# Optimization experiments

Hardware: AMD Instinct MI355X
Metric: run time of the kernel (lower is better)

## Reference

```python
import math
import jax, jax.numpy as jnp
import numpy as np

B, T, F = 2, 1024, 1024
H, DK, DV = 16, 64, 64
OUT = 1024


def _rel_shift_left(x):
    # x: (b, h, t1, t2); Transformer-XL left shift + tril mask (causal part)
    b, h, t1, t2 = x.shape
    xp = jnp.pad(x, ((0, 0), (0, 0), (0, 0), (1, 0)))
    xp = xp.reshape(b, h, t2 + 1, t1)[:, :, 1:].reshape(b, h, t1, t2)
    tril = jnp.tril(jnp.ones((t1, t2), x.dtype), t2 - t1)
    return xp * tril


def _rel_shift_right(x):
    # x: (b, h, t1, t2); right shift + triu mask (non-causal part)
    b, h, t1, t2 = x.shape
    xp = jnp.pad(x, ((0, 0), (0, 0), (0, 0), (0, 1)))
    xp = xp.reshape(b, h, t2 + 1, t1)[:, :, :-1].reshape(b, h, t1, t2)
    triu = jnp.triu(jnp.ones((t1, t2), x.dtype), t2 - t1 + 1)
    return xp * triu


def setup_inputs() -> dict:
    key = jax.random.key(0)
    ks = jax.random.split(key, 16)
    s = 0.02
    return {
        'query': jax.random.normal(ks[0], (B, T, F), jnp.float32),
        'key': jax.random.normal(ks[1], (B, T, F), jnp.float32),
        'value': jax.random.normal(ks[2], (B, T, F), jnp.float32),
        'pos_emb': jax.random.normal(ks[3], (1, T, F), jnp.float32),
        'Wq': jax.random.normal(ks[4], (H * DK, F), jnp.float32) * s,
        'bq': jnp.zeros((H * DK,), jnp.float32),
        'Wk': jax.random.normal(ks[5], (H * DK, F), jnp.float32) * s,
        'bk': jnp.zeros((H * DK,), jnp.float32),
        'Wv': jax.random.normal(ks[6], (H * DV, F), jnp.float32) * s,
        'bv': jnp.zeros((H * DV,), jnp.float32),
        'Wp': jax.random.normal(ks[7], (H * DK, F), jnp.float32) * s,
        'bp': jnp.zeros((H * DK,), jnp.float32),
        'Wo': jax.random.normal(ks[8], (OUT, H * DV), jnp.float32) * s,
        'bo': jnp.zeros((OUT,), jnp.float32),
        'u_bias': jax.random.normal(ks[9], (H, DK), jnp.float32) * s,
        'v_bias': jax.random.normal(ks[10], (H, DK), jnp.float32) * s,
    }


def reference(query, key, value, pos_emb, Wq, bq, Wk, bk, Wv, bv, Wp, bp, Wo, bo, u_bias, v_bias):
    b, t1, _ = query.shape
    t2 = key.shape[1]
    q = (query @ Wq.T + bq).reshape(b, t1, H, DK)          # (b, t1, h, dk)
    k = (key @ Wk.T + bk).reshape(b, t2, H, DK).transpose(0, 2, 1, 3)   # (b, h, t2, dk)
    v = (value @ Wv.T + bv).reshape(b, t2, H, DV).transpose(0, 2, 1, 3) # (b, h, t2, dv)
    p = (pos_emb @ Wp.T + bp).reshape(pos_emb.shape[0], -1, H, DK).transpose(0, 2, 1, 3)[0]  # (h, t2, dk)

    q_plus_u = (q + u_bias).transpose(0, 2, 1, 3)  # (b, h, t1, dk)
    q_plus_v = (q + v_bias).transpose(0, 2, 1, 3)  # (b, h, t1, dk)

    AC = jnp.einsum('bhtd,bhsd->bhts', q_plus_u, k)
    BD = _rel_shift_left(jnp.einsum('bhtd,hsd->bhts', q_plus_v, p))
    # non-causal part: flip pos embeddings along time, right shift
    BD = BD + _rel_shift_right(jnp.einsum('bhtd,hsd->bhts', q_plus_v, jnp.flip(p, axis=1)))

    scores = (AC + BD) / math.sqrt(DK)
    attn = jax.nn.softmax(scores, axis=-1)
    x = jnp.einsum('bhts,bhsd->bthd', attn, v).reshape(b, t1, H * DV)
    return x @ Wo.T + bo
```

## Files before the change

### kernel.cpp

```cpp
#include <hip/hip_runtime.h>
#include <hip/hip_bf16.h>
#include <stdint.h>

typedef __attribute__((ext_vector_type(8))) short bf16x8;
typedef __attribute__((ext_vector_type(4))) float f32x4;
typedef __attribute__((ext_vector_type(4))) short short4v;

#define SCALE2 0.18033688011112042f

__device__ __forceinline__ short f2b(float f) {
  union { float f; unsigned u; } un; un.f = f;
  unsigned r = un.u + 0x7FFFu + ((un.u >> 16) & 1u);
  return (short)(r >> 16);
}
__device__ __forceinline__ float b2f(short s) {
  union { unsigned u; float f; } un; un.u = ((unsigned)(unsigned short)s) << 16;
  return un.f;
}

#define GLDS(GP, LP) __builtin_amdgcn_global_load_lds( \
    (__attribute__((address_space(1))) void*)(GP), \
    (__attribute__((address_space(3))) void*)(LP), 16, 0, 0)

struct CvtTab { const float* s[12]; short* d[12]; };

__global__ void cvt_all(CvtTab tab) {
  int chunk = blockIdx.x >> 10;
  int off = (blockIdx.x & 1023) * 256 + threadIdx.x;
  float4 v = *((const float4*)tab.s[chunk] + off);
  short4v o;
  o[0] = f2b(v.x); o[1] = f2b(v.y); o[2] = f2b(v.z); o[3] = f2b(v.w);
  *((short4v*)tab.d[chunk] + off) = o;
}

__device__ __forceinline__ void gemm_core128(
    const short* __restrict__ A, const short* __restrict__ W,
    int tile_m, int tile_n, short* lds, f32x4 acc[4][4])
{
  const int tid = threadIdx.x;
  const int wave = tid >> 6, lane = tid & 63;
  const int wr = wave >> 1, wc = wave & 1;
  const int q15 = lane & 15, q4 = lane >> 4;
  const int rl = lane >> 3;
  const int cswz = ((lane & 7) * 16) ^ (rl << 4);

#pragma unroll
  for (int i = 0; i < 4; ++i)
#pragma unroll
    for (int j = 0; j < 4; ++j) acc[i][j] = (f32x4){0.f, 0.f, 0.f, 0.f};

  auto stage = [&](int buf, int k0) {
    short* As = lds + buf * 16384;
    short* Bs = As + 8192;
#pragma unroll
    for (int s = 0; s < 4; ++s) {
      int ia = wave * 4 + s;
      int row = ia * 8 + rl;
      GLDS(A + (size_t)(tile_m + row) * 1024 + k0 + (cswz >> 1), (char*)As + ia * 1024);
      GLDS(W + (size_t)(tile_n + row) * 1024 + k0 + (cswz >> 1), (char*)Bs + ia * 1024);
    }
  };

  stage(0, 0);
  __syncthreads();
  for (int t = 0; t < 16; ++t) {
    const int cur = t & 1;
    if (t < 15) stage(cur ^ 1, (t + 1) * 64);
    const short* As = lds + cur * 16384;
    const short* Bs = As + 8192;
#pragma unroll
    for (int kk = 0; kk < 2; ++kk) {
      const int kbyte = kk * 64 + q4 * 16;
      const int rswz = (q15 & 7) << 4;
      bf16x8 af[4], bfr[4];
#pragma unroll
      for (int i = 0; i < 4; ++i)
        af[i] = *(const bf16x8*)((const char*)As + (wr * 64 + i * 16 + q15) * 128 + (kbyte ^ rswz));
#pragma unroll
      for (int j = 0; j < 4; ++j)
        bfr[j] = *(const bf16x8*)((const char*)Bs + (wc * 64 + j * 16 + q15) * 128 + (kbyte ^ rswz));
#pragma unroll
      for (int i = 0; i < 4; ++i)
#pragma unroll
        for (int j = 0; j < 4; ++j)
          acc[i][j] = __builtin_amdgcn_mfma_f32_16x16x32_bf16(af[i], bfr[j], acc[i][j], 0, 0, 0);
    }
    __syncthreads();
  }
}

__global__ __launch_bounds__(256)
void gemm_qkvp(const short* __restrict__ q_in, const short* __restrict__ k_in,
               const short* __restrict__ v_in, const short* __restrict__ p_in,
               const short* __restrict__ wq, const short* __restrict__ wk,
               const short* __restrict__ wv, const short* __restrict__ wp,
               const float* __restrict__ bq, const float* __restrict__ bk,
               const float* __restrict__ bv, const float* __restrict__ bp,
               const float* __restrict__ ub, const float* __restrict__ vb,
               short* __restrict__ qu, short* __restrict__ qv,
               short* __restrict__ kx, short* __restrict__ vtp, short* __restrict__ pp)
{
  __shared__ __align__(16) short lds[32768];
  const int n = blockIdx.x;
  const int by = n & 7;
  const int bx = n >> 3;
  const short* A; const short* W; const float* bias; int tm, mode;
  if (bx < 16)      { A = q_in; W = wq; bias = bq; tm = bx;      mode = 0; }
  else if (bx < 32) { A = k_in; W = wk; bias = bk; tm = bx - 16; mode = 1; }
  else if (bx < 48) { A = v_in; W = wv; bias = bv; tm = bx - 32; mode = 2; }
  else              { A = p_in; W = wp; bias = bp; tm = bx - 48; mode = 3; }

  f32x4 acc[4][4];
  gemm_core128(A, W, tm * 128, by * 128, lds, acc);

  const int lane = threadIdx.x & 63, wave = threadIdx.x >> 6;
  const int wr = wave >> 1, wc = wave & 1, q15 = lane & 15, q4 = lane >> 4;
#pragma unroll
  for (int i = 0; i < 4; ++i)
#pragma unroll
    for (int j = 0; j < 4; ++j)
#pragma unroll
      for (int r = 0; r < 4; ++r) {
        int m = tm * 128 + wr * 64 + i * 16 + q4 * 4 + r;
        int nn = by * 128 + wc * 64 + j * 16 + q15;
        float v = acc[i][j][r] + bias[nn];
        int bb = m >> 10, t = m & 1023, hh = nn >> 6, d = nn & 63;
        if (mode == 0) {
          size_t o = ((size_t)(bb * 16 + hh) * 1024 + t) * 64 + d;
          qu[o] = f2b((v + ub[nn]) * SCALE2);
          qv[o] = f2b((v + vb[nn]) * SCALE2);
        } else if (mode == 1) {
          kx[((size_t)(bb * 16 + hh) * 1024 + t) * 64 + d] = f2b(v);
        } else if (mode == 2) {
          vtp[((size_t)(bb * 16 + hh) * 64 + d) * 1024 + t] = f2b(v);
        } else {
          pp[((size_t)hh * 1024 + m) * 64 + d] = f2b(v);
        }
      }
}

__global__ __launch_bounds__(256)
void gemm_out(const short* __restrict__ X, const short* __restrict__ W,
              const float* __restrict__ bo, float* __restrict__ out)
{
  __shared__ __align__(16) short lds[24576];
  const int n = blockIdx.x;
  const int bxm = (n >> 3) & 15;
  const int byn = ((n & 7) << 1) | (n >> 7);
  const int tile_m = bxm * 128, tile_n = byn * 64;

  const int tid = threadIdx.x;
  const int wave = tid >> 6, lane = tid & 63;
  const int wr = wave >> 1, wc = wave & 1;
  const int q15 = lane & 15, q4 = lane >> 4;
  const int rl = lane >> 3;
  const int cswz = ((lane & 7) * 16) ^ (rl << 4);

  f32x4 acc[4][2];
#pragma unroll
  for (int i = 0; i < 4; ++i)
#pragma unroll
    for (int j = 0; j < 2; ++j) acc[i][j] = (f32x4){0.f, 0.f, 0.f, 0.f};

  auto stage = [&](int buf, int k0) {
    short* As = lds + buf * 12288;
    short* Bs = As + 8192;
#pragma unroll
    for (int s = 0; s < 6; ++s) {
      int idx = wave * 6 + s;
      if (idx < 16) {
        int row = idx * 8 + rl;
        GLDS(X + (size_t)(tile_m + row) * 1024 + k0 + (cswz >> 1), (char*)As + idx * 1024);
      } else {
        int i2 = idx - 16;
        int row = i2 * 8 + rl;
        GLDS(W + (size_t)(tile_n + row) * 1024 + k0 + (cswz >> 1), (char*)Bs + i2 * 1024);
      }
    }
  };

  stage(0, 0);
  __syncthreads();
  for (int t = 0; t < 16; ++t) {
    const int cur = t & 1;
    if (t < 15) stage(cur ^ 1, (t + 1) * 64);
    const short* As = lds + cur * 12288;
    const short* Bs = As + 8192;
#pragma unroll
    for (int kk = 0; kk < 2; ++kk) {
      const int kbyte = kk * 64 + q4 * 16;
      const int rswz = (q15 & 7) << 4;
      bf16x8 af[4], bfr[2];
#pragma unroll
      for (int i = 0; i < 4; ++i)
        af[i] = *(const bf16x8*)((const char*)As + (wr * 64 + i * 16 + q15) * 128 + (kbyte ^ rswz));
#pragma unroll
      for (int j = 0; j < 2; ++j)
        bfr[j] = *(const bf16x8*)((const char*)Bs + (wc * 32 + j * 16 + q15) * 128 + (kbyte ^ rswz));
#pragma unroll
      for (int i = 0; i < 4; ++i)
#pragma unroll
        for (int j = 0; j < 2; ++j)
          acc[i][j] = __builtin_amdgcn_mfma_f32_16x16x32_bf16(af[i], bfr[j], acc[i][j], 0, 0, 0);
    }
    __syncthreads();
  }

#pragma unroll
  for (int i = 0; i < 4; ++i)
#pragma unroll
    for (int j = 0; j < 2; ++j)
#pragma unroll
      for (int r = 0; r < 4; ++r) {
        int m = tile_m + wr * 64 + i * 16 + q4 * 4 + r;
        int nn = tile_n + wc * 32 + j * 16 + q15;
        out[(size_t)m * 1024 + nn] = acc[i][j][r] + bo[nn];
      }
}

__global__ __launch_bounds__(256, 4)
void attn_kernel(const short* __restrict__ qu, const short* __restrict__ qv,
                 const short* __restrict__ kmat, const short* __restrict__ vt,
                 const short* __restrict__ p,
                 float* __restrict__ Opart, float* __restrict__ larr)
{
  __shared__ __align__(16) short Ks[4096];
  __shared__ __align__(16) short Vs[4096];
  __shared__ __align__(16) short Bl[4 * 2048];
  __shared__ __align__(16) short Pl[4 * 1024];

  const int nB = blockIdx.x;
  const int o = (nB & 7) * 128 + (nB >> 3);
  const int t0 = (o & 15) * 64;
  const int h = (o >> 4) & 15;
  const int z = o >> 8;
  const int b = z >> 1, sh = z & 1;

  const int tid = threadIdx.x;
  const int wave = tid >> 6, lane = tid & 63;
  const int q15 = lane & 15, q4 = lane >> 4;
  const size_t bh = (size_t)(b * 16 + h);
  const short* pW = p + (size_t)h * 65536;
  const int rswz = (q15 & 7) << 4;
  char* BlW = (char*)Bl + wave * 4096;
  char* PlW = (char*)Pl + wave * 2048;

  const int srow = tid >> 3;
  const int scol = (tid & 7) * 8;
  const int sdst = srow * 128 + ((scol * 2) ^ ((srow & 7) << 4));

  const int sbeg = sh * 512, send = sbeg + 512;
  const short* kg = kmat + (bh * 1024 + sbeg + srow) * 64 + scol;
  const short* vg = vt + (bh * 64 + srow) * 1024 + sbeg + scol;

  bf16x8 quf[2], qvf[2];
  {
    size_t base = (bh * 1024 + t0 + wave * 16 + q15) * 64 + q4 * 8;
    quf[0] = *(const bf16x8*)(qu + base);
    quf[1] = *(const bf16x8*)(qu + base + 32);
    qvf[0] = *(const bf16x8*)(qv + base);
    qvf[1] = *(const bf16x8*)(qv + base + 32);
  }

  f32x4 acco[4];
#pragma unroll
  for (int g = 0; g < 4; ++g) acco[g] = (f32x4){0.f, 0.f, 0.f, 0.f};
  float lrun[4] = {0.f, 0.f, 0.f, 0.f};

  int live0 = -1, live1 = -1;

  auto refill = [&](int base) {
    f32x4 bacc[4];
#pragma unroll
    for (int g = 0; g < 4; ++g) bacc[g] = (f32x4){0.f, 0.f, 0.f, 0.f};
#pragma unroll
    for (int kc = 0; kc < 2; ++kc) {
      const int kof = kc * 32 + q4 * 8;
#pragma unroll
      for (int g = 0; g < 4; ++g) {
        bf16x8 pf = *(const bf16x8*)(pW + (size_t)(base + g * 16 + q15) * 64 + kof);
        bacc[g] = __builtin_amdgcn_mfma_f32_16x16x32_bf16(qvf[kc], pf, bacc[g], 0, 0, 0);
      }
    }
#pragma unroll
    for (int g = 0; g < 4; ++g)
#pragma unroll
      for (int r = 0; r < 4; ++r) {
        int phys = ((base & 64) + g * 16 + q15 + q4 * 16) & 127;
        *(short*)(BlW + (q4 * 4 + r) * 256 + phys * 2) = f2b(bacc[g][r]);
      }
  };

  bf16x8 kr0 = *(const bf16x8*)kg;
  bf16x8 kr1 = *(const bf16x8*)(kg + 2048);
  bf16x8 vr0 = *(const bf16x8*)vg;
  bf16x8 vr1 = *(const bf16x8*)(vg + 32768);

  for (int s0 = sbeg; s0 < send; s0 += 64) {
    __syncthreads();
    *(bf16x8*)((char*)Ks + sdst) = kr0;
    *(bf16x8*)((char*)Ks + sdst + 4096) = kr1;
    *(bf16x8*)((char*)Vs + sdst) = vr0;
    *(bf16x8*)((char*)Vs + sdst + 4096) = vr1;
    __syncthreads();
    if (s0 + 64 < send) {
      kg += 4096; vg += 64;
      kr0 = *(const bf16x8*)kg;
      kr1 = *(const bf16x8*)(kg + 2048);
      vr0 = *(const bf16x8*)vg;
      vr1 = *(const bf16x8*)(vg + 32768);
    }

    f32x4 accac[4];
#pragma unroll
    for (int g = 0; g < 4; ++g) accac[g] = (f32x4){0.f, 0.f, 0.f, 0.f};
#pragma unroll
    for (int kc = 0; kc < 2; ++kc) {
      const int kbyte = kc * 64 + q4 * 16;
#pragma unroll
      for (int g = 0; g < 4; ++g) {
        bf16x8 kf = *(const bf16x8*)((const char*)Ks + (g * 16 + q15) * 128 + (kbyte ^ rswz));
        accac[g] = __builtin_amdgcn_mfma_f32_16x16x32_bf16(quf[kc], kf, accac[g], 0, 0, 0);
      }
    }

    const int dist0 = (t0 > s0) ? (t0 - s0) : (s0 - t0);
    const int jbase = 960 - dist0;
    {
      int sl = (jbase >> 6) & 1;
      bool nd = sl ? (live1 != jbase) : (live0 != jbase);
      if (nd) { refill(jbase); if (sl) live1 = jbase; else live0 = jbase; }
      int b1 = jbase + 64;
      if (b1 <= 960) {
        int sl1 = sl ^ 1;
        bool nd1 = sl1 ? (live1 != b1) : (live0 != b1);
        if (nd1) { refill(b1); if (sl1) live1 = b1; else live0 = b1; }
      }
    }

    const int rb = q4 * 1024;
    unsigned pb[4][4];
#define SCORE_ELEM(g, r, ARG) do {                                          \
      int aw = (ARG) & 127;                                                 \
      float bd = b2f(*(const short*)(BlW + rb + (r) * 256 + aw * 2));       \
      float e_ = exp2f(accac[g][r] + bd);                                   \
      unsigned t_ = __float_as_uint(e_) >> 16;                              \
      pb[g][r] = t_;                                                        \
      lrun[r] += __uint_as_float(t_ << 16);                                 \
    } while (0)

    if (s0 < t0) {
      const int C = 1023 - dist0 - wave * 16 + 12 * q4 + q15;
#pragma unroll
      for (int g = 0; g < 4; ++g)
#pragma unroll
        for (int r = 0; r < 4; ++r) SCORE_ELEM(g, r, C + 16 * g - r);
    } else if (s0 > t0) {
      const int C = 1023 - dist0 + wave * 16 + 20 * q4 - q15;
#pragma unroll
      for (int g = 0; g < 4; ++g)
#pragma unroll
        for (int r = 0; r < 4; ++r) SCORE_ELEM(g, r, C + r - 16 * g);
    } else {
      const int e0 = wave * 16 + 4 * q4 - q15;
      const int A = 1023 + 16 * q4;
#pragma unroll
      for (int g = 0; g < 4; ++g)
#pragma unroll
        for (int r = 0; r < 4; ++r) {
          int e = e0 + r - 16 * g;
          int d = e < 0 ? -e : e;
          SCORE_ELEM(g, r, A - d);
        }
    }
#undef SCORE_ELEM

#pragma unroll
    for (int g = 0; g < 4; ++g)
#pragma unroll
      for (int r = 0; r < 4; ++r) {
        int locR = q4 * 4 + r;
        *(short*)(PlW + locR * 128 + (((g * 16 + q15) * 2) ^ ((locR & 7) << 4))) = (short)pb[g][r];
      }

#pragma unroll
    for (int kc = 0; kc < 2; ++kc) {
      const int kbyte = kc * 64 + q4 * 16;
      bf16x8 pf = *(const bf16x8*)((const char*)PlW + q15 * 128 + (kbyte ^ rswz));
#pragma unroll
      for (int g = 0; g < 4; ++g) {
        bf16x8 vf = *(const bf16x8*)((const char*)Vs + (g * 16 + q15) * 128 + (kbyte ^ rswz));
        acco[g] = __builtin_amdgcn_mfma_f32_16x16x32_bf16(pf, vf, acco[g], 0, 0, 0);
      }
    }
  }

#pragma unroll
  for (int m = 1; m < 16; m <<= 1)
#pragma unroll
    for (int r = 0; r < 4; ++r) lrun[r] += __shfl_xor(lrun[r], m);

  size_t obase = ((size_t)(sh * 2 + b) * 16 + h) * 1024;
#pragma unroll
  for (int g = 0; g < 4; ++g)
#pragma unroll
    for (int r = 0; r < 4; ++r) {
      int tt = t0 + wave * 16 + q4 * 4 + r;
      Opart[(obase + tt) * 64 + g * 16 + q15] = acco[g][r];
    }
  if (q15 == 0)
#pragma unroll
    for (int r = 0; r < 4; ++r) {
      int tt = t0 + wave * 16 + q4 * 4 + r;
      larr[obase + tt] = lrun[r];
    }
}

__global__ void combine_k(const float* __restrict__ O, const float* __restrict__ larr,
                          short* __restrict__ x)
{
  int i = blockIdx.x * 256 + threadIdx.x;
  int dv4 = i & 15, rest = i >> 4;
  float4 a0 = *(const float4*)(O + (size_t)rest * 64 + dv4 * 4);
  float4 a1 = *(const float4*)(O + 2097152 + (size_t)rest * 64 + dv4 * 4);
  float l0 = larr[rest], l1 = larr[32768 + rest];
  float inv = 1.0f / (l0 + l1);
  int bq = rest >> 14, hq = (rest >> 10) & 15, tq = rest & 1023;
  short4v o;
  o[0] = f2b((a0.x + a1.x) * inv);
  o[1] = f2b((a0.y + a1.y) * inv);
  o[2] = f2b((a0.z + a1.z) * inv);
  o[3] = f2b((a0.w + a1.w) * inv);
  *(short4v*)(x + ((size_t)(bq * 1024 + tq) * 1024 + hq * 64 + dv4 * 4)) = o;
}

extern "C" void kernel_launch(void* const* d_in, const int* in_sizes, int n_in,
                              void* d_out, int out_size, void* d_ws, size_t ws_size,
                              hipStream_t stream) {
  const float* query = (const float*)d_in[0];
  const float* key   = (const float*)d_in[1];
  const float* value = (const float*)d_in[2];
  const float* pos   = (const float*)d_in[3];
  const float* Wq = (const float*)d_in[4];  const float* bq = (const float*)d_in[5];
  const float* Wk = (const float*)d_in[6];  const float* bk = (const float*)d_in[7];
  const float* Wv = (const float*)d_in[8];  const float* bv = (const float*)d_in[9];
  const float* Wp = (const float*)d_in[10]; const float* bp = (const float*)d_in[11];
  const float* Wo = (const float*)d_in[12]; const float* bo = (const float*)d_in[13];
  const float* ub = (const float*)d_in[14]; const float* vb = (const float*)d_in[15];

  char* ws = (char*)d_ws;
  const size_t MB = 1 << 20;
  short* Wo_bf    = (short*)(ws);
  short* qu_bf    = (short*)(ws + 2 * MB);
  short* qv_bf    = (short*)(ws + 6 * MB);
  short* k_bf     = (short*)(ws + 10 * MB);
  short* vT_bf    = (short*)(ws + 14 * MB);
  short* p_bf     = (short*)(ws + 18 * MB);
  short* x_bf     = (short*)(ws + 20 * MB);
  short* query_bf = (short*)(ws + 24 * MB);
  short* key_bf   = (short*)(ws + 28 * MB);
  short* value_bf = (short*)(ws + 32 * MB);
  short* pos_bf   = (short*)(ws + 36 * MB);
  short* Wq_bf    = (short*)(ws + 38 * MB);
  short* Wk_bf    = (short*)(ws + 40 * MB);
  short* Wv_bf    = (short*)(ws + 42 * MB);
  short* Wp_bf    = (short*)(ws + 44 * MB);
  float* Opart = (float*)(ws + 24 * MB);
  float* larr  = (float*)(ws + 40 * MB);

  CvtTab tab;
  tab.s[0] = query;           tab.d[0] = query_bf;
  tab.s[1] = query + 1048576; tab.d[1] = query_bf + 1048576;
  tab.s[2] = key;             tab.d[2] = key_bf;
  tab.s[3] = key + 1048576;   tab.d[3] = key_bf + 1048576;
  tab.s[4] = value;           tab.d[4] = value_bf;
  tab.s[5] = value + 1048576; tab.d[5] = value_bf + 1048576;
  tab.s[6] = pos;             tab.d[6] = pos_bf;
  tab.s[7] = Wq;              tab.d[7] = Wq_bf;
  tab.s[8] = Wk;              tab.d[8] = Wk_bf;
  tab.s[9] = Wv;              tab.d[9] = Wv_bf;
  tab.s[10] = Wp;             tab.d[10] = Wp_bf;
  tab.s[11] = Wo;             tab.d[11] = Wo_bf;
  hipLaunchKernelGGL(cvt_all, dim3(12288), dim3(256), 0, stream, tab);

  hipLaunchKernelGGL(gemm_qkvp, dim3(448), dim3(256), 0, stream,
                     query_bf, key_bf, value_bf, pos_bf,
                     Wq_bf, Wk_bf, Wv_bf, Wp_bf,
                     bq, bk, bv, bp, ub, vb,
                     qu_bf, qv_bf, k_bf, vT_bf, p_bf);

  hipLaunchKernelGGL(attn_kernel, dim3(1024), dim3(256), 0, stream,
                     qu_bf, qv_bf, k_bf, vT_bf, p_bf, Opart, larr);

  hipLaunchKernelGGL(combine_k, dim3(2048), dim3(256), 0, stream,
                     Opart, larr, x_bf);

  hipLaunchKernelGGL(gemm_out, dim3(256), dim3(256), 0, stream,
                     x_bf, Wo_bf, bo, (float*)d_out);
}
```

Baseline: 129.7 us.

## Transpose attention MFMA operands, vectorize BD/P LDS traffic, compute row sums via MFMA

Swaps the A/B operands of the score, BD-refill and PV MFMAs so each lane holds a query row across four consecutive key columns. This lets the BD table and P tile be written and read with packed 32/64-bit swizzled LDS accesses instead of per-element 16-bit ones. The softmax denominator is now accumulated by an extra MFMA against a ones vector, which removes the scalar per-element adds and the cross-lane shuffle reduction. The output is stored as float4 vectors, and s_setprio hints are wrapped around the MFMA sections. The new parity-based unaligned bf16 extraction adds ALU work and is a source of indexing risk.

Result: faster. 116.7 us (-10.0%).

```diff
diff --git a/kernel.cpp b/kernel.cpp
--- a/kernel.cpp
+++ b/kernel.cpp
@@ -5,6 +5,7 @@
 typedef __attribute__((ext_vector_type(8))) short bf16x8;
 typedef __attribute__((ext_vector_type(4))) float f32x4;
 typedef __attribute__((ext_vector_type(4))) short short4v;
+typedef __attribute__((ext_vector_type(2))) unsigned u32x2;
 
 #define SCALE2 0.18033688011112042f
 
@@ -12,10 +13,6 @@
   union { float f; unsigned u; } un; un.f = f;
   unsigned r = un.u + 0x7FFFu + ((un.u >> 16) & 1u);
   return (short)(r >> 16);
-}
-__device__ __forceinline__ float b2f(short s) {
-  union { unsigned u; float f; } un; un.u = ((unsigned)(unsigned short)s) << 16;
-  return un.f;
 }
 
 #define GLDS(GP, LP) __builtin_amdgcn_global_load_lds( \
@@ -226,8 +223,8 @@
 {
   __shared__ __align__(16) short Ks[4096];
   __shared__ __align__(16) short Vs[4096];
-  __shared__ __align__(16) short Bl[4 * 2048];
-  __shared__ __align__(16) short Pl[4 * 1024];
+  __shared__ __align__(16) short Bl[8192];
+  __shared__ __align__(16) short Pl[4096];
 
   const int nB = blockIdx.x;
   const int o = (nB & 7) * 128 + (nB >> 3);
@@ -244,6 +241,8 @@
   const int rswz = (q15 & 7) << 4;
   char* BlW = (char*)Bl + wave * 4096;
   char* PlW = (char*)Pl + wave * 2048;
+  const int blrow = q15 * 256;
+  const int plrow = q15 * 128;
 
   const int srow = tid >> 3;
   const int scol = (tid & 7) * 8;
@@ -261,11 +260,14 @@
     qvf[0] = *(const bf16x8*)(qv + base);
     qvf[1] = *(const bf16x8*)(qv + base + 32);
   }
-
-  f32x4 acco[4];
+  bf16x8 ones;
+#pragma unroll
+  for (int i = 0; i < 8; ++i) ones[i] = (short)0x3F80;
+
+  f32x4 acco[4], accl;
 #pragma unroll
   for (int g = 0; g < 4; ++g) acco[g] = (f32x4){0.f, 0.f, 0.f, 0.f};
-  float lrun[4] = {0.f, 0.f, 0.f, 0.f};
+  accl = (f32x4){0.f, 0.f, 0.f, 0.f};
 
   int live0 = -1, live1 = -1;
 
@@ -279,16 +281,22 @@
 #pragma unroll
       for (int g = 0; g < 4; ++g) {
         bf16x8 pf = *(const bf16x8*)(pW + (size_t)(base + g * 16 + q15) * 64 + kof);
-        bacc[g] = __builtin_amdgcn_mfma_f32_16x16x32_bf16(qvf[kc], pf, bacc[g], 0, 0, 0);
-      }
-    }
-#pragma unroll
-    for (int g = 0; g < 4; ++g)
-#pragma unroll
-      for (int r = 0; r < 4; ++r) {
-        int phys = ((base & 64) + g * 16 + q15 + q4 * 16) & 127;
-        *(short*)(BlW + (q4 * 4 + r) * 256 + phys * 2) = f2b(bacc[g][r]);
-      }
+        bacc[g] = __builtin_amdgcn_mfma_f32_16x16x32_bf16(pf, qvf[kc], bacc[g], 0, 0, 0);
+      }
+    }
+    const int pbase = base & 127;
+#pragma unroll
+    for (int g = 0; g < 4; ++g) {
+      unsigned a0 = __float_as_uint(bacc[g][0]); a0 = a0 + 0x7FFFu + ((a0 >> 16) & 1u);
+      unsigned a1 = __float_as_uint(bacc[g][1]); a1 = a1 + 0x7FFFu + ((a1 >> 16) & 1u);
+      unsigned a2 = __float_as_uint(bacc[g][2]); a2 = a2 + 0x7FFFu + ((a2 >> 16) & 1u);
+      unsigned a3 = __float_as_uint(bacc[g][3]); a3 = a3 + 0x7FFFu + ((a3 >> 16) & 1u);
+      u32x2 pk;
+      pk[0] = (a0 >> 16) | (a1 & 0xFFFF0000u);
+      pk[1] = (a2 >> 16) | (a3 & 0xFFFF0000u);
+      int inrow = (pbase + 16 * g + 4 * q4) * 2;
+      *(u32x2*)(BlW + blrow + (inrow ^ rswz)) = pk;
+    }
   };
 
   bf16x8 kr0 = *(const bf16x8*)kg;
@@ -314,15 +322,17 @@
     f32x4 accac[4];
 #pragma unroll
     for (int g = 0; g < 4; ++g) accac[g] = (f32x4){0.f, 0.f, 0.f, 0.f};
+    __builtin_amdgcn_s_setprio(1);
 #pragma unroll
     for (int kc = 0; kc < 2; ++kc) {
       const int kbyte = kc * 64 + q4 * 16;
 #pragma unroll
       for (int g = 0; g < 4; ++g) {
         bf16x8 kf = *(const bf16x8*)((const char*)Ks + (g * 16 + q15) * 128 + (kbyte ^ rswz));
-        accac[g] = __builtin_amdgcn_mfma_f32_16x16x32_bf16(quf[kc], kf, accac[g], 0, 0, 0);
-      }
-    }
+        accac[g] = __builtin_amdgcn_mfma_f32_16x16x32_bf16(kf, quf[kc], accac[g], 0, 0, 0);
+      }
+    }
+    __builtin_amdgcn_s_setprio(0);
 
     const int dist0 = (t0 > s0) ? (t0 - s0) : (s0 - t0);
     const int jbase = 960 - dist0;
@@ -337,83 +347,84 @@
         if (nd1) { refill(b1); if (sl1) live1 = b1; else live0 = b1; }
       }
     }
-
-    const int rb = q4 * 1024;
-    unsigned pb[4][4];
-#define SCORE_ELEM(g, r, ARG) do {                                          \
-      int aw = (ARG) & 127;                                                 \
-      float bd = b2f(*(const short*)(BlW + rb + (r) * 256 + aw * 2));       \
-      float e_ = exp2f(accac[g][r] + bd);                                   \
-      unsigned t_ = __float_as_uint(e_) >> 16;                              \
-      pb[g][r] = t_;                                                        \
-      lrun[r] += __uint_as_float(t_ << 16);                                 \
-    } while (0)
-
-    if (s0 < t0) {
-      const int C = 1023 - dist0 - wave * 16 + 12 * q4 + q15;
-#pragma unroll
-      for (int g = 0; g < 4; ++g)
-#pragma unroll
-        for (int r = 0; r < 4; ++r) SCORE_ELEM(g, r, C + 16 * g - r);
-    } else if (s0 > t0) {
-      const int C = 1023 - dist0 + wave * 16 + 20 * q4 - q15;
-#pragma unroll
-      for (int g = 0; g < 4; ++g)
-#pragma unroll
-        for (int r = 0; r < 4; ++r) SCORE_ELEM(g, r, C + r - 16 * g);
+    const int JB = jbase & 127;
+
+    unsigned pk01[4], pk23[4];
+    if (s0 != t0) {
+      const bool below = (s0 < t0);
+#pragma unroll
+      for (int g = 0; g < 4; ++g) {
+        int K = below ? (63 - 16 * wave - q15 + 16 * g + 4 * q4)
+                      : (60 + 16 * wave + q15 - 16 * g - 4 * q4);
+        int lo = JB + K;
+        int par = lo & 1;
+        int C = lo & ~1;
+        unsigned w0 = *(const unsigned*)(BlW + blrow + (((((C + 0) & 127) * 2)) ^ rswz));
+        unsigned w1 = *(const unsigned*)(BlW + blrow + (((((C + 2) & 127) * 2)) ^ rswz));
+        unsigned w2 = *(const unsigned*)(BlW + blrow + (((((C + 4) & 127) * 2)) ^ rswz));
+        unsigned u0 = par ? ((w1 << 16) | (w0 >> 16)) : w0;
+        unsigned u1 = par ? ((w2 << 16) | (w1 >> 16)) : w1;
+        float bd0, bd1, bd2, bd3;
+        if (below) {
+          bd0 = __uint_as_float(u0 << 16); bd1 = __uint_as_float(u0 & 0xFFFF0000u);
+          bd2 = __uint_as_float(u1 << 16); bd3 = __uint_as_float(u1 & 0xFFFF0000u);
+        } else {
+          bd3 = __uint_as_float(u0 << 16); bd2 = __uint_as_float(u0 & 0xFFFF0000u);
+          bd1 = __uint_as_float(u1 << 16); bd0 = __uint_as_float(u1 & 0xFFFF0000u);
+        }
+        float e0 = __builtin_amdgcn_exp2f(accac[g][0] + bd0);
+        float e1 = __builtin_amdgcn_exp2f(accac[g][1] + bd1);
+        float e2 = __builtin_amdgcn_exp2f(accac[g][2] + bd2);
+        float e3 = __builtin_amdgcn_exp2f(accac[g][3] + bd3);
+        pk01[g] = (__float_as_uint(e0) >> 16) | (__float_as_uint(e1) & 0xFFFF0000u);
+        pk23[g] = (__float_as_uint(e2) >> 16) | (__float_as_uint(e3) & 0xFFFF0000u);
+      }
     } else {
-      const int e0 = wave * 16 + 4 * q4 - q15;
-      const int A = 1023 + 16 * q4;
-#pragma unroll
-      for (int g = 0; g < 4; ++g)
+      const int tl = 16 * wave + q15;
+#pragma unroll
+      for (int g = 0; g < 4; ++g) {
+        float ev[4];
 #pragma unroll
         for (int r = 0; r < 4; ++r) {
-          int e = e0 + r - 16 * g;
+          int e = tl - (16 * g + 4 * q4 + r);
           int d = e < 0 ? -e : e;
-          SCORE_ELEM(g, r, A - d);
+          unsigned hv = *(const unsigned short*)(BlW + blrow + ((((127 - d) * 2)) ^ rswz));
+          float bd = __uint_as_float(hv << 16);
+          ev[r] = __builtin_amdgcn_exp2f(accac[g][r] + bd);
         }
-    }
-#undef SCORE_ELEM
-
-#pragma unroll
-    for (int g = 0; g < 4; ++g)
-#pragma unroll
-      for (int r = 0; r < 4; ++r) {
-        int locR = q4 * 4 + r;
-        *(short*)(PlW + locR * 128 + (((g * 16 + q15) * 2) ^ ((locR & 7) << 4))) = (short)pb[g][r];
-      }
-
+        pk01[g] = (__float_as_uint(ev[0]) >> 16) | (__float_as_uint(ev[1]) & 0xFFFF0000u);
+        pk23[g] = (__float_as_uint(ev[2]) >> 16) | (__float_as_uint(ev[3]) & 0xFFFF0000u);
+      }
+    }
+
+#pragma unroll
+    for (int g = 0; g < 4; ++g) {
+      u32x2 pk; pk[0] = pk01[g]; pk[1] = pk23[g];
+      int inrow = (16 * g + 4 * q4) * 2;
+      *(u32x2*)(PlW + plrow + (inrow ^ rswz)) = pk;
+    }
+
+    __builtin_amdgcn_s_setprio(1);
 #pragma unroll
     for (int kc = 0; kc < 2; ++kc) {
       const int kbyte = kc * 64 + q4 * 16;
-      bf16x8 pf = *(const bf16x8*)((const char*)PlW + q15 * 128 + (kbyte ^ rswz));
+      bf16x8 pf = *(const bf16x8*)(PlW + plrow + (kbyte ^ rswz));
+      accl = __builtin_amdgcn_mfma_f32_16x16x32_bf16(ones, pf, accl, 0, 0, 0);
 #pragma unroll
       for (int g = 0; g < 4; ++g) {
         bf16x8 vf = *(const bf16x8*)((const char*)Vs + (g * 16 + q15) * 128 + (kbyte ^ rswz));
-        acco[g] = __builtin_amdgcn_mfma_f32_16x16x32_bf16(pf, vf, acco[g], 0, 0, 0);
-      }
-    }
+        acco[g] = __builtin_amdgcn_mfma_f32_16x16x32_bf16(vf, pf, acco[g], 0, 0, 0);
+      }
+    }
+    __builtin_amdgcn_s_setprio(0);
   }
 
-#pragma unroll
-  for (int m = 1; m < 16; m <<= 1)
-#pragma unroll
-    for (int r = 0; r < 4; ++r) lrun[r] += __shfl_xor(lrun[r], m);
-
   size_t obase = ((size_t)(sh * 2 + b) * 16 + h) * 1024;
+  const int tt = t0 + wave * 16 + q15;
 #pragma unroll
   for (int g = 0; g < 4; ++g)
-#pragma unroll
-    for (int r = 0; r < 4; ++r) {
-      int tt = t0 + wave * 16 + q4 * 4 + r;
-      Opart[(obase + tt) * 64 + g * 16 + q15] = acco[g][r];
-    }
-  if (q15 == 0)
-#pragma unroll
-    for (int r = 0; r < 4; ++r) {
-      int tt = t0 + wave * 16 + q4 * 4 + r;
-      larr[obase + tt] = lrun[r];
-    }
+    *(f32x4*)(Opart + (obase + tt) * 64 + 16 * g + 4 * q4) = acco[g];
+  if (lane < 16) larr[obase + tt] = accl[0];
 }
 
 __global__ void combine_k(const float* __restrict__ O, const float* __restrict__ larr,
```
